# Kernel optimization log

Hardware: AMD Instinct MI355X
Metric: run time of the kernel (lower is better)

## Reference

```python
import jax, jax.numpy as jnp
import numpy as np

B, S, H = 1, 1024, 2880
NQ, NKV, D = 64, 8, 64          # query heads, kv heads, head_dim
G = NQ // NKV                    # GQA group size
W = 128                          # sliding window
SCALE = D ** -0.5
NEG = -1e30


def rotate_half(x):
    x1, x2 = jnp.split(x, 2, axis=-1)
    return jnp.concatenate((-x2, x1), axis=-1)


def setup_inputs() -> dict:
    key = jax.random.key(0)
    ks = jax.random.split(key, 8)
    hidden_states = jax.random.normal(ks[0], (B, S, H), jnp.float32)
    # rotary tables, half head_dim (module concats (cos,cos) to full dim)
    pos = jnp.arange(S, dtype=jnp.float32)[:, None]
    inv = 1.0 / (10000.0 ** (jnp.arange(0, D, 2, dtype=jnp.float32) / D))
    ang = pos * inv[None, :]                      # (S, D/2)
    cos = jnp.cos(ang)[None].astype(jnp.float32)  # (1, S, D/2)
    sin = jnp.sin(ang)[None].astype(jnp.float32)
    w_qkv = jax.random.normal(ks[1], (H, (NQ + 2 * NKV) * D), jnp.float32) * 0.02
    b_qkv = jax.random.normal(ks[2], ((NQ + 2 * NKV) * D,), jnp.float32) * 0.02
    w_o = jax.random.normal(ks[3], (NQ * D, H), jnp.float32) * 0.02
    b_o = jax.random.normal(ks[4], (H,), jnp.float32) * 0.02
    sinks = jax.random.normal(ks[5], (NQ,), jnp.float32)
    k_cache = jnp.zeros((B, S, NKV, D), jnp.float32)
    v_cache = jnp.zeros((B, S, NKV, D), jnp.float32)
    return {"hidden_states": hidden_states, "cos": cos, "sin": sin,
            "w_qkv": w_qkv, "b_qkv": b_qkv, "w_o": w_o, "b_o": b_o,
            "sinks": sinks, "k_cache": k_cache, "v_cache": v_cache, "kv_len": 0}


def reference(hidden_states, cos, sin, w_qkv, b_qkv, w_o, b_o, sinks,
              k_cache, v_cache, kv_len):
    # fused QKV projection + split
    qkv = hidden_states @ w_qkv + b_qkv                      # (B, S, (NQ+2*NKV)*D)
    q, k, v = jnp.split(qkv, [NQ * D, NQ * D + NKV * D], axis=-1)
    q = q.reshape(B, S, NQ, D)
    k = k.reshape(B, S, NKV, D)
    v = v.reshape(B, S, NKV, D)
    # RoPE (BSND layout, half-dim tables duplicated to full dim)
    cosf = jnp.concatenate((cos, cos), axis=-1)[:, :, None, :]
    sinf = jnp.concatenate((sin, sin), axis=-1)[:, :, None, :]
    q = q * cosf + rotate_half(q) * sinf
    k = k * cosf + rotate_half(k) * sinf
    # KV-cache scatter update at position kv_len along seq dim
    k_cache = jax.lax.dynamic_update_slice(k_cache, k, (0, kv_len, 0, 0))
    v_cache = jax.lax.dynamic_update_slice(v_cache, v, (0, kv_len, 0, 0))
    T = kv_len + S
    keys = k_cache[:, :T]                                    # (B, T, NKV, D)
    vals = v_cache[:, :T]
    # GQA: group query heads by kv head
    qg = q.reshape(B, S, NKV, G, D)
    scores = jnp.einsum('bqhgd,bkhd->bhgqk', qg, keys) * SCALE  # (B,NKV,G,S,T)
    # causal + sliding-window mask
    i = jnp.arange(S)[:, None] + kv_len
    j = jnp.arange(T)[None, :]
    allowed = (j <= i) & (i - j < W)
    scores = jnp.where(allowed, scores, NEG)
    # softmax with per-head learnable sink logit (sink gets no value)
    sk = sinks.reshape(NKV, G)[None, :, :, None]             # (1,NKV,G,1)
    m = jnp.maximum(jnp.max(scores, axis=-1), sk)            # (B,NKV,G,S)
    p = jnp.exp(scores - m[..., None])
    denom = jnp.sum(p, axis=-1) + jnp.exp(sk - m)
    attn = jnp.einsum('bhgqk,bkhd->bqhgd', p / denom[..., None], vals)
    out = attn.reshape(B, S, NQ * D) @ w_o + b_o             # (B, S, H)
    return out
```

## Files before the change

### kernel.cpp

```cpp
#include <hip/hip_runtime.h>
#include <hip/hip_bf16.h>

#define NQH 64
#define NKVH 8
#define DH 64
#define SEQ 1024
#define HID 2880
#define QKV_N 5120
#define ATTN_N 4096
#define WIN 128
#define WO_NPAD 2944
#define SCALE_F 0.125f

typedef __attribute__((ext_vector_type(8))) __bf16 bf16x8;
typedef __attribute__((ext_vector_type(4))) float f32x4;

#define GLOAD_LDS16(g, l) \
    __builtin_amdgcn_global_load_lds((const __attribute__((address_space(1))) void*)(g), \
                                     (__attribute__((address_space(3))) void*)(l), 16, 0, 0)

__device__ __forceinline__ ushort f2bf(float x) {
    union { float f; unsigned int u; } c; c.f = x;
    unsigned int u = c.u;
    unsigned int r = (u + 0x7FFFu + ((u >> 16) & 1u)) >> 16;
    return (ushort)r;
}

__global__ __launch_bounds__(256) void convert_f32_bf16(
    const float* __restrict__ in, ushort* __restrict__ out, int n4)
{
    int idx = blockIdx.x * blockDim.x + threadIdx.x;
    int stride = gridDim.x * blockDim.x;
    for (int i = idx; i < n4; i += stride) {
        float4 v = reinterpret_cast<const float4*>(in)[i];
        ushort4 o;
        o.x = f2bf(v.x); o.y = f2bf(v.y); o.z = f2bf(v.z); o.w = f2bf(v.w);
        reinterpret_cast<ushort4*>(out)[i] = o;
    }
}

__global__ __launch_bounds__(256) void transpose_convert(
    const float* __restrict__ in, ushort* __restrict__ out, int K, int N)
{
    __shared__ ushort tile[64][80];
    const int bk = blockIdx.x * 64;
    const int bn = blockIdx.y * 64;
    const int tid = threadIdx.x;
    const bool inb = bn < N;

#pragma unroll
    for (int it = 0; it < 4; ++it) {
        int r = it * 16 + (tid >> 4);
        int c4 = (tid & 15) * 4;
        float4 v = make_float4(0.f, 0.f, 0.f, 0.f);
        if (inb) v = *(const float4*)&in[(size_t)(bk + r) * N + bn + c4];
        tile[c4 + 0][r] = f2bf(v.x);
        tile[c4 + 1][r] = f2bf(v.y);
        tile[c4 + 2][r] = f2bf(v.z);
        tile[c4 + 3][r] = f2bf(v.w);
    }
    __syncthreads();
#pragma unroll
    for (int it = 0; it < 2; ++it) {
        int nr = it * 32 + (tid >> 3);
        int c8 = (tid & 7) * 8;
        uint4 v = *(const uint4*)&tile[nr][c8];
        *(uint4*)&out[(size_t)(bn + nr) * K + bk + c8] = v;
    }
}

template<bool ROPE>
__global__ __launch_bounds__(256) void gemm64x128(
    const ushort* __restrict__ A, const ushort* __restrict__ BT,
    const float* __restrict__ bias, float* __restrict__ C,
    int K, int ldC, int Nreal,
    const float* __restrict__ cosp, const float* __restrict__ sinp)
{
    __shared__ ushort Al[64 * 64];
    __shared__ ushort Bl[128 * 64];
    const int t = threadIdx.x;
    const int lane = t & 63;
    const int w = t >> 6;
    const int wr = w >> 1, wc = w & 1;
    const int g4 = lane >> 4;
    const int r15 = lane & 15;

    const int flat = blockIdx.x + gridDim.x * blockIdx.y;
    const int per = (gridDim.x * gridDim.y) >> 3;
    const int virt = (flat & 7) * per + (flat >> 3);
    const int m0 = (virt & 15) * 64;
    const int n0 = (virt >> 4) * 128;

    const ushort* aSrc0; const ushort* aSrc1;
    ushort* aDst0; ushort* aDst1;
    {
        int lin0 = t, lin1 = 256 + t;
        int row0 = lin0 >> 3, row1 = lin1 >> 3;
        int ch0 = (lin0 & 7) ^ (row0 & 7);
        int ch1 = (lin1 & 7) ^ (row1 & 7);
        aSrc0 = A + (size_t)(m0 + row0) * K + ch0 * 8;
        aSrc1 = A + (size_t)(m0 + row1) * K + ch1 * 8;
        aDst0 = &Al[lin0 * 8];
        aDst1 = &Al[lin1 * 8];
    }
    const ushort* bSrc[4]; ushort* bDst[4];
#pragma unroll
    for (int i = 0; i < 4; ++i) {
        int lin = i * 256 + t;
        int col = lin >> 3;
        int ch = (lin & 7) ^ (col & 7);
        bSrc[i] = BT + (size_t)(n0 + col) * K + ch * 8;
        bDst[i] = &Bl[lin * 8];
    }

    int aoff[2][2], boff[4][2];
#pragma unroll
    for (int mi = 0; mi < 2; ++mi)
#pragma unroll
        for (int ks = 0; ks < 2; ++ks) {
            int row = wr * 32 + mi * 16 + r15;
            int slot = (ks * 4 + g4) ^ (row & 7);
            aoff[mi][ks] = row * 64 + slot * 8;
        }
#pragma unroll
    for (int ni = 0; ni < 4; ++ni)
#pragma unroll
        for (int ks = 0; ks < 2; ++ks) {
            int col = wc * 64 + ni * 16 + r15;
            int slot = (ks * 4 + g4) ^ (col & 7);
            boff[ni][ks] = col * 64 + slot * 8;
        }

    f32x4 acc[2][4];
#pragma unroll
    for (int mi = 0; mi < 2; ++mi)
#pragma unroll
        for (int ni = 0; ni < 4; ++ni) acc[mi][ni] = (f32x4){0.f, 0.f, 0.f, 0.f};

    for (int k0 = 0; k0 < K; k0 += 64) {
        GLOAD_LDS16(aSrc0, aDst0);
        GLOAD_LDS16(aSrc1, aDst1);
        GLOAD_LDS16(bSrc[0], bDst[0]);
        GLOAD_LDS16(bSrc[1], bDst[1]);
        GLOAD_LDS16(bSrc[2], bDst[2]);
        GLOAD_LDS16(bSrc[3], bDst[3]);
        aSrc0 += 64; aSrc1 += 64;
        bSrc[0] += 64; bSrc[1] += 64; bSrc[2] += 64; bSrc[3] += 64;
        __syncthreads();
#pragma unroll
        for (int ks = 0; ks < 2; ++ks) {
            bf16x8 a0 = *(const bf16x8*)&Al[aoff[0][ks]];
            bf16x8 a1 = *(const bf16x8*)&Al[aoff[1][ks]];
            bf16x8 b0 = *(const bf16x8*)&Bl[boff[0][ks]];
            bf16x8 b1 = *(const bf16x8*)&Bl[boff[1][ks]];
            bf16x8 b2 = *(const bf16x8*)&Bl[boff[2][ks]];
            bf16x8 b3 = *(const bf16x8*)&Bl[boff[3][ks]];
            acc[0][0] = __builtin_amdgcn_mfma_f32_16x16x32_bf16(a0, b0, acc[0][0], 0, 0, 0);
            acc[0][1] = __builtin_amdgcn_mfma_f32_16x16x32_bf16(a0, b1, acc[0][1], 0, 0, 0);
            acc[0][2] = __builtin_amdgcn_mfma_f32_16x16x32_bf16(a0, b2, acc[0][2], 0, 0, 0);
            acc[0][3] = __builtin_amdgcn_mfma_f32_16x16x32_bf16(a0, b3, acc[0][3], 0, 0, 0);
            acc[1][0] = __builtin_amdgcn_mfma_f32_16x16x32_bf16(a1, b0, acc[1][0], 0, 0, 0);
            acc[1][1] = __builtin_amdgcn_mfma_f32_16x16x32_bf16(a1, b1, acc[1][1], 0, 0, 0);
            acc[1][2] = __builtin_amdgcn_mfma_f32_16x16x32_bf16(a1, b2, acc[1][2], 0, 0, 0);
            acc[1][3] = __builtin_amdgcn_mfma_f32_16x16x32_bf16(a1, b3, acc[1][3], 0, 0, 0);
        }
        __syncthreads();
    }

    float vals[2][4][4];
#pragma unroll
    for (int ni = 0; ni < 4; ++ni) {
        int col = n0 + wc * 64 + ni * 16 + r15;
        float bv = (col < Nreal) ? bias[col] : 0.f;
#pragma unroll
        for (int mi = 0; mi < 2; ++mi)
#pragma unroll
            for (int r = 0; r < 4; ++r) vals[mi][ni][r] = acc[mi][ni][r] + bv;
    }
    if (ROPE) {
        const int head = (n0 + wc * 64) >> 6;
        if (head < 72) {
#pragma unroll
            for (int mi = 0; mi < 2; ++mi)
#pragma unroll
                for (int r = 0; r < 4; ++r) {
                    int q = m0 + wr * 32 + mi * 16 + g4 * 4 + r;
#pragma unroll
                    for (int dp = 0; dp < 2; ++dp) {
                        int d = dp * 16 + r15;
                        float c = cosp[q * 32 + d];
                        float s = sinp[q * 32 + d];
                        float x1 = vals[mi][dp][r];
                        float x2 = vals[mi][dp + 2][r];
                        vals[mi][dp][r]     = x1 * c - x2 * s;
                        vals[mi][dp + 2][r] = x2 * c + x1 * s;
                    }
                }
        }
    }
#pragma unroll
    for (int ni = 0; ni < 4; ++ni) {
        int col = n0 + wc * 64 + ni * 16 + r15;
        if (col < Nreal) {
#pragma unroll
            for (int mi = 0; mi < 2; ++mi) {
                int row = m0 + wr * 32 + mi * 16 + g4 * 4;
#pragma unroll
                for (int r = 0; r < 4; ++r)
                    C[(size_t)(row + r) * ldC + col] = vals[mi][ni][r];
            }
        }
    }
}

__global__ __launch_bounds__(512) void attn_mfma_kernel(
    const float* __restrict__ qkv, const float* __restrict__ sinks,
    ushort* __restrict__ attn_out)
{
    __shared__ __align__(16) ushort Kl[160][72];
    __shared__ __align__(16) ushort Vt[64][168];
    __shared__ __align__(16) ushort Pl[8][32][40];
    const int t = threadIdx.x;
    const int w = t >> 6;
    const int l = t & 63;
    const int g4 = l >> 4;
    const int r15 = l & 15;
    const int q0 = blockIdx.x * 32;
    const int hk = blockIdx.y;
    const int kbase = q0 - 128;

#pragma unroll
    for (int i = 0; i < 5; ++i) {
        int idx = i * 512 + t;
        int row = idx >> 4;
        int c4 = (idx & 15) * 4;
        int j = kbase + row;
        float4 kv = make_float4(0.f, 0.f, 0.f, 0.f);
        float4 vv = make_float4(0.f, 0.f, 0.f, 0.f);
        if (j >= 0) {
            kv = *(const float4*)&qkv[(size_t)j * QKV_N + 4096 + hk * 64 + c4];
            vv = *(const float4*)&qkv[(size_t)j * QKV_N + 4608 + hk * 64 + c4];
        }
        ushort4 kp;
        kp.x = f2bf(kv.x); kp.y = f2bf(kv.y); kp.z = f2bf(kv.z); kp.w = f2bf(kv.w);
        *(ushort4*)&Kl[row][c4] = kp;
        Vt[c4 + 0][row] = f2bf(vv.x);
        Vt[c4 + 1][row] = f2bf(vv.y);
        Vt[c4 + 2][row] = f2bf(vv.z);
        Vt[c4 + 3][row] = f2bf(vv.w);
    }

    bf16x8 qf[2][2];
#pragma unroll
    for (int ct = 0; ct < 2; ++ct) {
        int R = w * 32 + ct * 16 + r15;
        int q = q0 + (R & 31);
        int hq = hk * 8 + (R >> 5);
        const float* qb = &qkv[(size_t)q * QKV_N + hq * 64];
#pragma unroll
        for (int s = 0; s < 2; ++s) {
            float4 a = *(const float4*)&qb[s * 32 + g4 * 8];
            float4 b = *(const float4*)&qb[s * 32 + g4 * 8 + 4];
            union { ushort u[8]; bf16x8 v; } pk;
            pk.u[0] = f2bf(a.x * SCALE_F); pk.u[1] = f2bf(a.y * SCALE_F);
            pk.u[2] = f2bf(a.z * SCALE_F); pk.u[3] = f2bf(a.w * SCALE_F);
            pk.u[4] = f2bf(b.x * SCALE_F); pk.u[5] = f2bf(b.y * SCALE_F);
            pk.u[6] = f2bf(b.z * SCALE_F); pk.u[7] = f2bf(b.w * SCALE_F);
            qf[ct][s] = pk.v;
        }
    }
    __syncthreads();

    f32x4 sc[10][2];
#pragma unroll
    for (int kt = 0; kt < 10; ++kt) {
        sc[kt][0] = (f32x4){0.f, 0.f, 0.f, 0.f};
        sc[kt][1] = (f32x4){0.f, 0.f, 0.f, 0.f};
    }
#pragma unroll
    for (int kt = 0; kt < 10; ++kt) {
#pragma unroll
        for (int s = 0; s < 2; ++s) {
            bf16x8 kf = *(const bf16x8*)&Kl[kt * 16 + r15][s * 32 + g4 * 8];
            sc[kt][0] = __builtin_amdgcn_mfma_f32_16x16x32_bf16(kf, qf[0][s], sc[kt][0], 0, 0, 0);
            sc[kt][1] = __builtin_amdgcn_mfma_f32_16x16x32_bf16(kf, qf[1][s], sc[kt][1], 0, 0, 0);
        }
    }

    const int minkey = 128 - q0;
#pragma unroll
    for (int ct = 0; ct < 2; ++ct) {
        int R = w * 32 + ct * 16 + r15;
        int ql = R & 31;
        float snk = sinks[hk * 8 + (R >> 5)];
#pragma unroll
        for (int kt = 0; kt < 10; ++kt)
#pragma unroll
            for (int r = 0; r < 4; ++r) {
                int key = kt * 16 + g4 * 4 + r;
                bool ok = (key > ql) && (key <= ql + 128) && (key >= minkey);
                if (!ok) sc[kt][ct][r] = -1e30f;
            }
        float m = snk;
#pragma unroll
        for (int kt = 0; kt < 10; ++kt)
#pragma unroll
            for (int r = 0; r < 4; ++r) m = fmaxf(m, sc[kt][ct][r]);
        m = fmaxf(m, __shfl_xor(m, 16));
        m = fmaxf(m, __shfl_xor(m, 32));
        float sum = 0.f;
#pragma unroll
        for (int kt = 0; kt < 10; ++kt)
#pragma unroll
            for (int r = 0; r < 4; ++r) {
                float p = __expf(sc[kt][ct][r] - m);
                sc[kt][ct][r] = p;
                sum += p;
            }
        sum += __shfl_xor(sum, 16);
        sum += __shfl_xor(sum, 32);
        sum += __expf(snk - m);
        float iv = 1.0f / sum;
#pragma unroll
        for (int kt = 0; kt < 10; ++kt)
#pragma unroll
            for (int r = 0; r < 4; ++r) sc[kt][ct][r] *= iv;
    }

    f32x4 pv[2][4];
#pragma unroll
    for (int mi = 0; mi < 2; ++mi)
#pragma unroll
        for (int ni = 0; ni < 4; ++ni) pv[mi][ni] = (f32x4){0.f, 0.f, 0.f, 0.f};

#pragma unroll
    for (int s = 0; s < 5; ++s) {
#pragma unroll
        for (int ct = 0; ct < 2; ++ct)
#pragma unroll
            for (int kh = 0; kh < 2; ++kh) {
                int kt = 2 * s + kh;
                ushort4 p4;
                p4.x = f2bf(sc[kt][ct][0]);
                p4.y = f2bf(sc[kt][ct][1]);
                p4.z = f2bf(sc[kt][ct][2]);
                p4.w = f2bf(sc[kt][ct][3]);
                *(ushort4*)&Pl[w][ct * 16 + r15][kh * 16 + g4 * 4] = p4;
            }
#pragma unroll
        for (int mi = 0; mi < 2; ++mi) {
            bf16x8 pf = *(const bf16x8*)&Pl[w][mi * 16 + r15][g4 * 8];
#pragma unroll
            for (int ni = 0; ni < 4; ++ni) {
                bf16x8 vf = *(const bf16x8*)&Vt[ni * 16 + r15][s * 32 + g4 * 8];
                pv[mi][ni] = __builtin_amdgcn_mfma_f32_16x16x32_bf16(pf, vf, pv[mi][ni], 0, 0, 0);
            }
        }
    }

#pragma unroll
    for (int mi = 0; mi < 2; ++mi)
#pragma unroll
        for (int r = 0; r < 4; ++r) {
            int R = w * 32 + mi * 16 + g4 * 4 + r;
            int q = q0 + (R & 31);
            int hq = hk * 8 + (R >> 5);
            ushort* ob = &attn_out[(size_t)q * ATTN_N + hq * 64 + r15];
#pragma unroll
            for (int ni = 0; ni < 4; ++ni)
                ob[ni * 16] = f2bf(pv[mi][ni][r]);
        }
}

extern "C" void kernel_launch(void* const* d_in, const int* in_sizes, int n_in,
                              void* d_out, int out_size, void* d_ws, size_t ws_size,
                              hipStream_t stream)
{
    const float* hidden = (const float*)d_in[0];
    const float* cosp   = (const float*)d_in[1];
    const float* sinp   = (const float*)d_in[2];
    const float* w_qkv  = (const float*)d_in[3];
    const float* b_qkv  = (const float*)d_in[4];
    const float* w_o    = (const float*)d_in[5];
    const float* b_o    = (const float*)d_in[6];
    const float* sinks  = (const float*)d_in[7];

    char* ws = (char*)d_ws;
    size_t off = 0;
    ushort* wqkvT = (ushort*)(ws + off); off += (size_t)QKV_N * HID * 2;
    ushort* woT   = (ushort*)(ws + off); off += (size_t)WO_NPAD * ATTN_N * 2;
    float*  qkv   = (float*)(ws + off);  off += (size_t)SEQ * QKV_N * 4;
    ushort* hidden_b = (ushort*)(ws + off);
    ushort* attn_b   = (ushort*)(ws + off); off += (size_t)SEQ * ATTN_N * 2;
    if (off > ws_size) return;

    transpose_convert<<<dim3(HID / 64, QKV_N / 64), 256, 0, stream>>>(w_qkv, wqkvT, HID, QKV_N);
    transpose_convert<<<dim3(ATTN_N / 64, WO_NPAD / 64), 256, 0, stream>>>(w_o, woT, ATTN_N, HID);
    convert_f32_bf16<<<2048, 256, 0, stream>>>(hidden, hidden_b, SEQ * HID / 4);

    gemm64x128<true><<<dim3(QKV_N / 128, SEQ / 64), 256, 0, stream>>>(
        hidden_b, wqkvT, b_qkv, qkv, HID, QKV_N, QKV_N, cosp, sinp);

    attn_mfma_kernel<<<dim3(SEQ / 32, NKVH), 512, 0, stream>>>(qkv, sinks, attn_b);

    gemm64x128<false><<<dim3(WO_NPAD / 128, SEQ / 64), 256, 0, stream>>>(
        attn_b, woT, b_o, (float*)d_out, ATTN_N, HID, HID, nullptr, nullptr);
}
```

Baseline: 147.9 us.

## Double-buffer LDS tiles in GEMM to overlap global loads with MFMA

```diff
diff --git a/kernel.cpp b/kernel.cpp
--- a/kernel.cpp
+++ b/kernel.cpp
@@ -76,8 +76,8 @@
     int K, int ldC, int Nreal,
     const float* __restrict__ cosp, const float* __restrict__ sinp)
 {
-    __shared__ ushort Al[64 * 64];
-    __shared__ ushort Bl[128 * 64];
+    __shared__ ushort Al[2 * 64 * 64];
+    __shared__ ushort Bl[2 * 128 * 64];
     const int t = threadIdx.x;
     const int lane = t & 63;
     const int w = t >> 6;
@@ -103,15 +103,26 @@
         aDst0 = &Al[lin0 * 8];
         aDst1 = &Al[lin1 * 8];
     }
-    const ushort* bSrc[4]; ushort* bDst[4];
-#pragma unroll
-    for (int i = 0; i < 4; ++i) {
-        int lin = i * 256 + t;
-        int col = lin >> 3;
-        int ch = (lin & 7) ^ (col & 7);
-        bSrc[i] = BT + (size_t)(n0 + col) * K + ch * 8;
-        bDst[i] = &Bl[lin * 8];
-    }
+    const ushort* bSrc0; const ushort* bSrc1; const ushort* bSrc2; const ushort* bSrc3;
+    ushort* bDst0; ushort* bDst1; ushort* bDst2; ushort* bDst3;
+    {
+        int lin;
+        lin = t;       bSrc0 = BT + (size_t)(n0 + (lin >> 3)) * K + (((lin & 7) ^ ((lin >> 3) & 7)) * 8); bDst0 = &Bl[lin * 8];
+        lin = 256 + t; bSrc1 = BT + (size_t)(n0 + (lin >> 3)) * K + (((lin & 7) ^ ((lin >> 3) & 7)) * 8); bDst1 = &Bl[lin * 8];
+        lin = 512 + t; bSrc2 = BT + (size_t)(n0 + (lin >> 3)) * K + (((lin & 7) ^ ((lin >> 3) & 7)) * 8); bDst2 = &Bl[lin * 8];
+        lin = 768 + t; bSrc3 = BT + (size_t)(n0 + (lin >> 3)) * K + (((lin & 7) ^ ((lin >> 3) & 7)) * 8); bDst3 = &Bl[lin * 8];
+    }
+
+#define STAGE_TILE(bufsel) do { \
+        GLOAD_LDS16(aSrc0, aDst0 + (bufsel) * 4096); \
+        GLOAD_LDS16(aSrc1, aDst1 + (bufsel) * 4096); \
+        GLOAD_LDS16(bSrc0, bDst0 + (bufsel) * 8192); \
+        GLOAD_LDS16(bSrc1, bDst1 + (bufsel) * 8192); \
+        GLOAD_LDS16(bSrc2, bDst2 + (bufsel) * 8192); \
+        GLOAD_LDS16(bSrc3, bDst3 + (bufsel) * 8192); \
+        aSrc0 += 64; aSrc1 += 64; \
+        bSrc0 += 64; bSrc1 += 64; bSrc2 += 64; bSrc3 += 64; \
+    } while (0)
 
     int aoff[2][2], boff[4][2];
 #pragma unroll
@@ -137,35 +148,43 @@
 #pragma unroll
         for (int ni = 0; ni < 4; ++ni) acc[mi][ni] = (f32x4){0.f, 0.f, 0.f, 0.f};
 
-    for (int k0 = 0; k0 < K; k0 += 64) {
-        GLOAD_LDS16(aSrc0, aDst0);
-        GLOAD_LDS16(aSrc1, aDst1);
-        GLOAD_LDS16(bSrc[0], bDst[0]);
-        GLOAD_LDS16(bSrc[1], bDst[1]);
-        GLOAD_LDS16(bSrc[2], bDst[2]);
-        GLOAD_LDS16(bSrc[3], bDst[3]);
-        aSrc0 += 64; aSrc1 += 64;
-        bSrc[0] += 64; bSrc[1] += 64; bSrc[2] += 64; bSrc[3] += 64;
+#define COMPUTE_TILE(bufsel) do { \
+        const ushort* Ab = &Al[(bufsel) * 4096]; \
+        const ushort* Bb = &Bl[(bufsel) * 8192]; \
+        _Pragma("unroll") \
+        for (int ks = 0; ks < 2; ++ks) { \
+            bf16x8 a0 = *(const bf16x8*)&Ab[aoff[0][ks]]; \
+            bf16x8 a1 = *(const bf16x8*)&Ab[aoff[1][ks]]; \
+            bf16x8 b0 = *(const bf16x8*)&Bb[boff[0][ks]]; \
+            bf16x8 b1 = *(const bf16x8*)&Bb[boff[1][ks]]; \
+            bf16x8 b2 = *(const bf16x8*)&Bb[boff[2][ks]]; \
+            bf16x8 b3 = *(const bf16x8*)&Bb[boff[3][ks]]; \
+            acc[0][0] = __builtin_amdgcn_mfma_f32_16x16x32_bf16(a0, b0, acc[0][0], 0, 0, 0); \
+            acc[0][1] = __builtin_amdgcn_mfma_f32_16x16x32_bf16(a0, b1, acc[0][1], 0, 0, 0); \
+            acc[0][2] = __builtin_amdgcn_mfma_f32_16x16x32_bf16(a0, b2, acc[0][2], 0, 0, 0); \
+            acc[0][3] = __builtin_amdgcn_mfma_f32_16x16x32_bf16(a0, b3, acc[0][3], 0, 0, 0); \
+            acc[1][0] = __builtin_amdgcn_mfma_f32_16x16x32_bf16(a1, b0, acc[1][0], 0, 0, 0); \
+            acc[1][1] = __builtin_amdgcn_mfma_f32_16x16x32_bf16(a1, b1, acc[1][1], 0, 0, 0); \
+            acc[1][2] = __builtin_amdgcn_mfma_f32_16x16x32_bf16(a1, b2, acc[1][2], 0, 0, 0); \
+            acc[1][3] = __builtin_amdgcn_mfma_f32_16x16x32_bf16(a1, b3, acc[1][3], 0, 0, 0); \
+        } \
+    } while (0)
+
+    const int NT = K >> 6;
+    STAGE_TILE(0);
+    __syncthreads();
+    for (int kt = 0; kt < NT; kt += 2) {
+        if (kt + 1 < NT) STAGE_TILE(1);
+        COMPUTE_TILE(0);
         __syncthreads();
-#pragma unroll
-        for (int ks = 0; ks < 2; ++ks) {
-            bf16x8 a0 = *(const bf16x8*)&Al[aoff[0][ks]];
-            bf16x8 a1 = *(const bf16x8*)&Al[aoff[1][ks]];
-            bf16x8 b0 = *(const bf16x8*)&Bl[boff[0][ks]];
-            bf16x8 b1 = *(const bf16x8*)&Bl[boff[1][ks]];
-            bf16x8 b2 = *(const bf16x8*)&Bl[boff[2][ks]];
-            bf16x8 b3 = *(const bf16x8*)&Bl[boff[3][ks]];
-            acc[0][0] = __builtin_amdgcn_mfma_f32_16x16x32_bf16(a0, b0, acc[0][0], 0, 0, 0);
-            acc[0][1] = __builtin_amdgcn_mfma_f32_16x16x32_bf16(a0, b1, acc[0][1], 0, 0, 0);
-            acc[0][2] = __builtin_amdgcn_mfma_f32_16x16x32_bf16(a0, b2, acc[0][2], 0, 0, 0);
-            acc[0][3] = __builtin_amdgcn_mfma_f32_16x16x32_bf16(a0, b3, acc[0][3], 0, 0, 0);
-            acc[1][0] = __builtin_amdgcn_mfma_f32_16x16x32_bf16(a1, b0, acc[1][0], 0, 0, 0);
-            acc[1][1] = __builtin_amdgcn_mfma_f32_16x16x32_bf16(a1, b1, acc[1][1], 0, 0, 0);
-            acc[1][2] = __builtin_amdgcn_mfma_f32_16x16x32_bf16(a1, b2, acc[1][2], 0, 0, 0);
-            acc[1][3] = __builtin_amdgcn_mfma_f32_16x16x32_bf16(a1, b3, acc[1][3], 0, 0, 0);
-        }
-        __syncthreads();
-    }
+        if (kt + 1 < NT) {
+            if (kt + 2 < NT) STAGE_TILE(0);
+            COMPUTE_TILE(1);
+            __syncthreads();
+        }
+    }
+#undef STAGE_TILE
+#undef COMPUTE_TILE
 
     float vals[2][4][4];
 #pragma unroll
```

Measured after the change: 147.9 us. No clear change (+0.0%).
